# Kernel tuning notes

Measured on AMD Instinct MI355X. Metric: run time of the kernel, lower is better.

Reference implementation:

```python
import jax, jax.numpy as jnp
import numpy as np

N_NODES = 102400
N_EDGES = 1638400
DIMS = [128, 64, 32, 1]  # decoder_dim=128, decoder_l=3, last layer -> 1


def setup_inputs() -> dict:
    key = jax.random.key(0)
    ks = jax.random.split(key, 10)
    inp = {
        'b_z': jax.random.normal(ks[0], (N_NODES, DIMS[0]), jnp.float32),
        'src': jax.random.randint(ks[1], (N_EDGES,), 0, N_NODES, jnp.int64 if jax.config.jax_enable_x64 else jnp.int32),
        'dst': jax.random.randint(ks[2], (N_EDGES,), 0, N_NODES, jnp.int64 if jax.config.jax_enable_x64 else jnp.int32),
        'edge_weight': jax.random.uniform(ks[3], (N_EDGES,), jnp.float32),
        'b_size': 100,
    }
    # GraphConv weights: W [in, out], bias [out] (DGL xavier init; randn ok for ref)
    for i in range(3):
        inp[f'W{i}'] = jax.random.normal(ks[4 + i], (DIMS[i], DIMS[i + 1]), jnp.float32) * (1.0 / np.sqrt(DIMS[i]))
        inp[f'b{i}'] = jnp.zeros((DIMS[i + 1],), jnp.float32)
    return inp


def _gcn_layer(h, src, dst, ew, W, b, activate):
    n = h.shape[0]
    ones = jnp.ones((src.shape[0],), h.dtype)
    # norm='both': symmetric degree normalization with plain (unweighted) degrees
    out_deg = jnp.clip(jax.ops.segment_sum(ones, src, num_segments=n), 1.0)
    in_deg = jnp.clip(jax.ops.segment_sum(ones, dst, num_segments=n), 1.0)
    h = h * (out_deg ** -0.5)[:, None]
    h = h @ W  # in_feats > out_feats: transform before aggregation (DGL order)
    msg = h[src] * ew[:, None]           # [E, out] edge-weighted gather
    agg = jax.ops.segment_sum(msg, dst, num_segments=n)  # scatter-add
    agg = agg * (in_deg ** -0.5)[:, None] + b
    return jnp.tanh(agg) if activate else agg


def reference(b_z, src, dst, edge_weight, b_size, W0, b0, W1, b1, W2, b2):
    h = b_z
    h = _gcn_layer(h, src, dst, edge_weight, W0, b0, True)
    h = _gcn_layer(h, src, dst, edge_weight, W1, b1, True)
    h = _gcn_layer(h, src, dst, edge_weight, W2, b2, False)
    return h.reshape(b_size, -1)
```

## Files before the change

### kernel.cpp

```cpp
#include <hip/hip_runtime.h>
#include <hip/hip_fp16.h>
#include <math.h>

#define N_NODES 102400
#define N_EDGES 1638400
#define NB 100
#define PB 256
#define EPB (N_EDGES/PB)

union H4 { int2 i2; __half h[4]; };

__global__ __launch_bounds__(256) void histA_kernel(const int* __restrict__ src, const int* __restrict__ dst,
                                                    int* __restrict__ histD, int* __restrict__ histS) {
    __shared__ int hD[NB], hS[NB];
    int tid = threadIdx.x;
    if (tid < NB) { hD[tid] = 0; hS[tid] = 0; }
    __syncthreads();
    int base = blockIdx.x * EPB;
    for (int i = tid; i < EPB; i += 256) {
        atomicAdd(&hD[dst[base + i] >> 10], 1);
        atomicAdd(&hS[src[base + i] >> 10], 1);
    }
    __syncthreads();
    if (tid < NB) {
        histD[blockIdx.x * NB + tid] = hD[tid];
        histS[blockIdx.x * NB + tid] = hS[tid];
    }
}

__global__ __launch_bounds__(256) void scanB_kernel(const int* __restrict__ histD, const int* __restrict__ histS,
                                                    int* __restrict__ offD, int* __restrict__ offS,
                                                    int* __restrict__ coarseD, int* __restrict__ coarseS) {
    __shared__ int totD[NB], totS[NB], baseD[NB + 1], baseS[NB + 1];
    int t = threadIdx.x;
    if (t < NB) { int s = 0; for (int k = 0; k < PB; k++) s += histD[k * NB + t]; totD[t] = s; }
    else if (t >= 128 && t < 128 + NB) { int j = t - 128; int s = 0; for (int k = 0; k < PB; k++) s += histS[k * NB + j]; totS[j] = s; }
    __syncthreads();
    if (t == 0)   { int r = 0; for (int j = 0; j < NB; j++) { baseD[j] = r; r += totD[j]; } baseD[NB] = r; }
    if (t == 128) { int r = 0; for (int j = 0; j < NB; j++) { baseS[j] = r; r += totS[j]; } baseS[NB] = r; }
    __syncthreads();
    if (t < NB) { int r = baseD[t]; for (int k = 0; k < PB; k++) { offD[k * NB + t] = r; r += histD[k * NB + t]; } }
    else if (t >= 128 && t < 128 + NB) { int j = t - 128; int r = baseS[j]; for (int k = 0; k < PB; k++) { offS[k * NB + j] = r; r += histS[k * NB + j]; } }
    if (t <= NB) coarseD[t] = baseD[t];
    if (t >= 128 && t <= 128 + NB) coarseS[t - 128] = baseS[t - 128];
}

__global__ __launch_bounds__(256) void partC_kernel(const int* __restrict__ src, const int* __restrict__ dst,
                                                    const float* __restrict__ ew,
                                                    const int* __restrict__ offD, const int* __restrict__ offS,
                                                    int2* __restrict__ partD, unsigned short* __restrict__ partS) {
    __shared__ int cD[NB], cS[NB];
    int tid = threadIdx.x;
    if (tid < NB) { cD[tid] = offD[blockIdx.x * NB + tid]; cS[tid] = offS[blockIdx.x * NB + tid]; }
    __syncthreads();
    int base = blockIdx.x * EPB;
    for (int i = tid; i < EPB; i += 256) {
        int s = src[base + i], d = dst[base + i];
        float w = ew[base + i];
        int p = atomicAdd(&cD[d >> 10], 1);
        partD[p] = make_int2(s | ((d & 1023) << 17), __float_as_int(w));
        int q = atomicAdd(&cS[s >> 10], 1);
        partS[q] = (unsigned short)(s & 1023);
    }
}

__global__ __launch_bounds__(1024) void fineS_kernel(const unsigned short* __restrict__ partS, const int* __restrict__ coarseS,
                                                     float* __restrict__ outdeg_inv) {
    __shared__ int hist[1024];
    int tid = threadIdx.x;
    hist[tid] = 0;
    __syncthreads();
    int beg = coarseS[blockIdx.x], end = coarseS[blockIdx.x + 1];
    for (int i = beg + tid; i < end; i += 1024) atomicAdd(&hist[partS[i]], 1);
    __syncthreads();
    outdeg_inv[blockIdx.x * 1024 + tid] = 1.0f / sqrtf((float)max(hist[tid], 1));
}

__global__ __launch_bounds__(1024) void fineD_kernel(const int2* __restrict__ partD, const int* __restrict__ coarseD,
                                                     const float* __restrict__ outdeg_inv,
                                                     int2* __restrict__ edge_perm, int* __restrict__ row_off,
                                                     float* __restrict__ indeg_inv) {
    __shared__ int hist[1024], cursor[1024];
    __shared__ int wsum[16];
    int tid = threadIdx.x, lane = tid & 63, wid = tid >> 6;
    hist[tid] = 0;
    __syncthreads();
    int beg = coarseD[blockIdx.x], end = coarseD[blockIdx.x + 1];
    for (int i = beg + tid; i < end; i += 1024) atomicAdd(&hist[(partD[i].x >> 17) & 1023], 1);
    __syncthreads();
    int v = hist[tid];
    int x = v;
    #pragma unroll
    for (int s = 1; s < 64; s <<= 1) { int t = __shfl_up(x, s, 64); if (lane >= s) x += t; }
    if (lane == 63) wsum[wid] = x;
    __syncthreads();
    if (wid == 0) {
        int ws = (lane < 16) ? wsum[lane] : 0;
        int y = ws;
        #pragma unroll
        for (int s = 1; s < 16; s <<= 1) { int t = __shfl_up(y, s, 64); if (lane >= s) y += t; }
        if (lane < 16) wsum[lane] = y - ws;
    }
    __syncthreads();
    int ex = wsum[wid] + x - v;
    cursor[tid] = beg + ex;
    int node = blockIdx.x * 1024 + tid;
    row_off[node] = beg + ex;
    indeg_inv[node] = 1.0f / sqrtf((float)max(v, 1));
    if (blockIdx.x == NB - 1 && tid == 0) row_off[N_NODES] = N_EDGES;
    __syncthreads();
    for (int i = beg + tid; i < end; i += 1024) {
        int2 t2 = partD[i];
        int d = (t2.x >> 17) & 1023, s = t2.x & 0x1FFFF;
        int p = atomicAdd(&cursor[d], 1);
        float w = __int_as_float(t2.y) * outdeg_inv[s];
        edge_perm[p] = make_int2(s, __float_as_int(w));
    }
}

template<int K, int C, int RN>
__global__ __launch_bounds__(256) void gemm_tile_kernel(
    const float* __restrict__ h, const float* __restrict__ W, __half* __restrict__ out) {
    constexpr int BM = 64;
    constexpr int RM = 4;
    constexpr int KC = 64;
    constexpr int TX = C / RN;
    constexpr int TY = BM / RM;
    static_assert(TX * TY == 256, "bad tile");
    static_assert(RN == 4, "fp16 epilogue assumes RN==4");

    __shared__ float Ws[K * C];
    __shared__ float Hs[KC][BM + 4];

    const int tid = threadIdx.x;
    const long brow = (long)blockIdx.x * BM;

    for (int i = tid; i < K * C; i += 256) Ws[i] = W[i];

    const int tx = tid % TX;
    const int ty = tid / TX;
    float acc[RM][RN] = {};

    const int lr = tid % 16;
    const int lk = tid / 16;

    for (int kc = 0; kc < K; kc += KC) {
        __syncthreads();
        #pragma unroll
        for (int p0 = 0; p0 < BM; p0 += 16) {
            const int r = p0 + lr;
            const float4 hv = *(const float4*)(h + (brow + r) * K + kc + lk * 4);
            Hs[lk * 4 + 0][r] = hv.x;
            Hs[lk * 4 + 1][r] = hv.y;
            Hs[lk * 4 + 2][r] = hv.z;
            Hs[lk * 4 + 3][r] = hv.w;
        }
        __syncthreads();

        #pragma unroll
        for (int k = 0; k < KC; ++k) {
            const float4 a4 = *(const float4*)&Hs[k][ty * RM];
            const float av[RM] = {a4.x, a4.y, a4.z, a4.w};
            float b[RN];
            *(float4*)b = *(const float4*)&Ws[(kc + k) * C + tx * RN];
            #pragma unroll
            for (int i = 0; i < RM; ++i)
                #pragma unroll
                for (int j = 0; j < RN; ++j)
                    acc[i][j] += av[i] * b[j];
        }
    }

    #pragma unroll
    for (int i = 0; i < RM; ++i) {
        const long row = brow + ty * RM + i;
        __half2 p01 = __floats2half2_rn(acc[i][0], acc[i][1]);
        __half2 p23 = __floats2half2_rn(acc[i][2], acc[i][3]);
        int2 packed = make_int2(*(int*)&p01, *(int*)&p23);
        *(int2*)(out + row * C + tx * RN) = packed;
    }
}

__global__ __launch_bounds__(256) void agg64_gemm_kernel(
    const __half* __restrict__ ht, const int* __restrict__ row_off,
    const int2* __restrict__ ep, const float* __restrict__ indeg_inv,
    const float* __restrict__ b0, const float* __restrict__ W1,
    __half* __restrict__ ht1, int N) {
    __shared__ float h1s[8][64];
    const int tid = threadIdx.x;
    const int lane = tid & 63;
    const int wv = tid >> 6;
    const int chunk = lane & 15;
    const int eslot = lane >> 4;
    const int hf = lane >> 5;
    const int c = lane & 31;

    float w1reg[32];
    #pragma unroll
    for (int j = 0; j < 32; ++j) w1reg[j] = W1[(hf * 32 + j) * 32 + c];
    const float bch = b0[(chunk << 2) | eslot];
    const char* htb = (const char*)ht;
    const unsigned coff = (unsigned)(chunk << 3);

    const int pair0 = (blockIdx.x * blockDim.x + tid) >> 6;
    const int npairs = N >> 1;
    const int nwaves = (gridDim.x * blockDim.x) >> 6;

    for (int pid = pair0; pid < npairs; pid += nwaves) {
        const int n0 = pid << 1;
        const int ro0 = row_off[n0], ro1 = row_off[n0 + 1], ro2 = row_off[n0 + 2];
        const int em0 = max(ro1 - 1, 0), em1 = max(ro2 - 1, 0);
        float4 a0 = {0, 0, 0, 0}, a1 = {0, 0, 0, 0};
        float4 c0 = {0, 0, 0, 0}, c1 = {0, 0, 0, 0};
        int e0 = ro0, e1 = ro1;
        while (true) {
            const int i00 = e0 + eslot, i01 = i00 + 4, i02 = i00 + 8, i03 = i00 + 12;
            const int j00 = e1 + eslot, j01 = j00 + 4, j02 = j00 + 8, j03 = j00 + 12;
            int2 p00 = ep[min(i00, em0)];
            int2 p01 = ep[min(i01, em0)];
            int2 p02 = ep[min(i02, em0)];
            int2 p03 = ep[min(i03, em0)];
            int2 p10 = ep[min(j00, em1)];
            int2 p11 = ep[min(j01, em1)];
            int2 p12 = ep[min(j02, em1)];
            int2 p13 = ep[min(j03, em1)];
            float w00 = (i00 < ro1) ? __int_as_float(p00.y) : 0.0f;
            float w01 = (i01 < ro1) ? __int_as_float(p01.y) : 0.0f;
            float w02 = (i02 < ro1) ? __int_as_float(p02.y) : 0.0f;
            float w03 = (i03 < ro1) ? __int_as_float(p03.y) : 0.0f;
            float w10 = (j00 < ro2) ? __int_as_float(p10.y) : 0.0f;
            float w11 = (j01 < ro2) ? __int_as_float(p11.y) : 0.0f;
            float w12 = (j02 < ro2) ? __int_as_float(p12.y) : 0.0f;
            float w13 = (j03 < ro2) ? __int_as_float(p13.y) : 0.0f;
            H4 r00, r01, r02, r03, r10, r11, r12, r13;
            r00.i2 = *(const int2*)(htb + (((unsigned)p00.x << 7) | coff));
            r01.i2 = *(const int2*)(htb + (((unsigned)p01.x << 7) | coff));
            r02.i2 = *(const int2*)(htb + (((unsigned)p02.x << 7) | coff));
            r03.i2 = *(const int2*)(htb + (((unsigned)p03.x << 7) | coff));
            r10.i2 = *(const int2*)(htb + (((unsigned)p10.x << 7) | coff));
            r11.i2 = *(const int2*)(htb + (((unsigned)p11.x << 7) | coff));
            r12.i2 = *(const int2*)(htb + (((unsigned)p12.x << 7) | coff));
            r13.i2 = *(const int2*)(htb + (((unsigned)p13.x << 7) | coff));
            a0.x = fmaf(__half2float(r00.h[0]), w00, a0.x);
            a0.y = fmaf(__half2float(r00.h[1]), w00, a0.y);
            a0.z = fmaf(__half2float(r00.h[2]), w00, a0.z);
            a0.w = fmaf(__half2float(r00.h[3]), w00, a0.w);
            a1.x = fmaf(__half2float(r01.h[0]), w01, a1.x);
            a1.y = fmaf(__half2float(r01.h[1]), w01, a1.y);
            a1.z = fmaf(__half2float(r01.h[2]), w01, a1.z);
            a1.w = fmaf(__half2float(r01.h[3]), w01, a1.w);
            a0.x = fmaf(__half2float(r02.h[0]), w02, a0.x);
            a0.y = fmaf(__half2float(r02.h[1]), w02, a0.y);
            a0.z = fmaf(__half2float(r02.h[2]), w02, a0.z);
            a0.w = fmaf(__half2float(r02.h[3]), w02, a0.w);
            a1.x = fmaf(__half2float(r03.h[0]), w03, a1.x);
            a1.y = fmaf(__half2float(r03.h[1]), w03, a1.y);
            a1.z = fmaf(__half2float(r03.h[2]), w03, a1.z);
            a1.w = fmaf(__half2float(r03.h[3]), w03, a1.w);
            c0.x = fmaf(__half2float(r10.h[0]), w10, c0.x);
            c0.y = fmaf(__half2float(r10.h[1]), w10, c0.y);
            c0.z = fmaf(__half2float(r10.h[2]), w10, c0.z);
            c0.w = fmaf(__half2float(r10.h[3]), w10, c0.w);
            c1.x = fmaf(__half2float(r11.h[0]), w11, c1.x);
            c1.y = fmaf(__half2float(r11.h[1]), w11, c1.y);
            c1.z = fmaf(__half2float(r11.h[2]), w11, c1.z);
            c1.w = fmaf(__half2float(r11.h[3]), w11, c1.w);
            c0.x = fmaf(__half2float(r12.h[0]), w12, c0.x);
            c0.y = fmaf(__half2float(r12.h[1]), w12, c0.y);
            c0.z = fmaf(__half2float(r12.h[2]), w12, c0.z);
            c0.w = fmaf(__half2float(r12.h[3]), w12, c0.w);
            c1.x = fmaf(__half2float(r13.h[0]), w13, c1.x);
            c1.y = fmaf(__half2float(r13.h[1]), w13, c1.y);
            c1.z = fmaf(__half2float(r13.h[2]), w13, c1.z);
            c1.w = fmaf(__half2float(r13.h[3]), w13, c1.w);
            e0 += 16; e1 += 16;
            if (e0 >= ro1 && e1 >= ro2) break;
        }
        a0.x += a1.x; a0.y += a1.y; a0.z += a1.z; a0.w += a1.w;
        c0.x += c1.x; c0.y += c1.y; c0.z += c1.z; c0.w += c1.w;
        #pragma unroll
        for (int s = 16; s <= 32; s <<= 1) {
            a0.x += __shfl_xor(a0.x, s, 64);
            a0.y += __shfl_xor(a0.y, s, 64);
            a0.z += __shfl_xor(a0.z, s, 64);
            a0.w += __shfl_xor(a0.w, s, 64);
            c0.x += __shfl_xor(c0.x, s, 64);
            c0.y += __shfl_xor(c0.y, s, 64);
            c0.z += __shfl_xor(c0.z, s, 64);
            c0.w += __shfl_xor(c0.w, s, 64);
        }
        const float sc0 = indeg_inv[n0], sc1 = indeg_inv[n0 + 1];
        float v0 = (eslot == 0) ? a0.x : (eslot == 1) ? a0.y : (eslot == 2) ? a0.z : a0.w;
        float v1 = (eslot == 0) ? c0.x : (eslot == 1) ? c0.y : (eslot == 2) ? c0.z : c0.w;
        v0 = tanhf(fmaf(v0, sc0, bch));
        v1 = tanhf(fmaf(v1, sc1, bch));
        const int sl = wv << 1;
        h1s[sl][(chunk << 2) | eslot] = v0;
        h1s[sl + 1][(chunk << 2) | eslot] = v1;
        asm volatile("s_waitcnt lgkmcnt(0)" ::: "memory");
        float t0 = 0.0f, t1 = 0.0f;
        #pragma unroll
        for (int j4 = 0; j4 < 8; ++j4) {
            const float4 h0 = *(const float4*)&h1s[sl][hf * 32 + j4 * 4];
            const float4 h1 = *(const float4*)&h1s[sl + 1][hf * 32 + j4 * 4];
            t0 = fmaf(h0.x, w1reg[j4 * 4 + 0], t0);
            t0 = fmaf(h0.y, w1reg[j4 * 4 + 1], t0);
            t0 = fmaf(h0.z, w1reg[j4 * 4 + 2], t0);
            t0 = fmaf(h0.w, w1reg[j4 * 4 + 3], t0);
            t1 = fmaf(h1.x, w1reg[j4 * 4 + 0], t1);
            t1 = fmaf(h1.y, w1reg[j4 * 4 + 1], t1);
            t1 = fmaf(h1.z, w1reg[j4 * 4 + 2], t1);
            t1 = fmaf(h1.w, w1reg[j4 * 4 + 3], t1);
        }
        t0 += __shfl_xor(t0, 32, 64);
        t1 += __shfl_xor(t1, 32, 64);
        if (hf == 0) {
            ht1[(long)n0 * 32 + c] = __float2half_rn(t0);
            ht1[(long)(n0 + 1) * 32 + c] = __float2half_rn(t1);
        }
    }
}

__global__ __launch_bounds__(256) void agg32_dot_kernel(const __half* __restrict__ ht, const int* __restrict__ row_off,
                                 const int2* __restrict__ ep,
                                 const float* __restrict__ indeg_inv, const float* __restrict__ bias,
                                 const float* __restrict__ W2, float* __restrict__ ht2, int N) {
    int pid = (blockIdx.x * blockDim.x + threadIdx.x) >> 6;
    int lane = threadIdx.x & 63;
    int n0 = pid << 1;
    if (n0 >= N) return;
    int chunk = lane & 7;
    int eslot = lane >> 3;
    int ro0 = row_off[n0], ro1 = row_off[n0 + 1], ro2 = row_off[n0 + 2];
    int em0 = max(ro1 - 1, 0), em1 = max(ro2 - 1, 0);
    const char* htb = (const char*)ht;
    unsigned coff = (unsigned)(chunk << 3);
    float4 a0 = {0, 0, 0, 0}, a1 = {0, 0, 0, 0};
    float4 c0 = {0, 0, 0, 0}, c1 = {0, 0, 0, 0};
    int e0 = ro0, e1 = ro1;
    while (true) {
        int i00 = e0 + eslot, i01 = i00 + 8;
        int j00 = e1 + eslot, j01 = j00 + 8;
        int2 p00 = ep[min(i00, em0)];
        int2 p01 = ep[min(i01, em0)];
        int2 p10 = ep[min(j00, em1)];
        int2 p11 = ep[min(j01, em1)];
        float w00 = (i00 < ro1) ? __int_as_float(p00.y) : 0.0f;
        float w01 = (i01 < ro1) ? __int_as_float(p01.y) : 0.0f;
        float w10 = (j00 < ro2) ? __int_as_float(p10.y) : 0.0f;
        float w11 = (j01 < ro2) ? __int_as_float(p11.y) : 0.0f;
        H4 r00, r01, r10, r11;
        r00.i2 = *(const int2*)(htb + (((unsigned)p00.x << 6) | coff));
        r01.i2 = *(const int2*)(htb + (((unsigned)p01.x << 6) | coff));
        r10.i2 = *(const int2*)(htb + (((unsigned)p10.x << 6) | coff));
        r11.i2 = *(const int2*)(htb + (((unsigned)p11.x << 6) | coff));
        a0.x = fmaf(__half2float(r00.h[0]), w00, a0.x);
        a0.y = fmaf(__half2float(r00.h[1]), w00, a0.y);
        a0.z = fmaf(__half2float(r00.h[2]), w00, a0.z);
        a0.w = fmaf(__half2float(r00.h[3]), w00, a0.w);
        a1.x = fmaf(__half2float(r01.h[0]), w01, a1.x);
        a1.y = fmaf(__half2float(r01.h[1]), w01, a1.y);
        a1.z = fmaf(__half2float(r01.h[2]), w01, a1.z);
        a1.w = fmaf(__half2float(r01.h[3]), w01, a1.w);
        c0.x = fmaf(__half2float(r10.h[0]), w10, c0.x);
        c0.y = fmaf(__half2float(r10.h[1]), w10, c0.y);
        c0.z = fmaf(__half2float(r10.h[2]), w10, c0.z);
        c0.w = fmaf(__half2float(r10.h[3]), w10, c0.w);
        c1.x = fmaf(__half2float(r11.h[0]), w11, c1.x);
        c1.y = fmaf(__half2float(r11.h[1]), w11, c1.y);
        c1.z = fmaf(__half2float(r11.h[2]), w11, c1.z);
        c1.w = fmaf(__half2float(r11.h[3]), w11, c1.w);
        e0 += 16; e1 += 16;
        if (e0 >= ro1 && e1 >= ro2) break;
    }
    a0.x += a1.x; a0.y += a1.y; a0.z += a1.z; a0.w += a1.w;
    c0.x += c1.x; c0.y += c1.y; c0.z += c1.z; c0.w += c1.w;
    #pragma unroll
    for (int s = 8; s <= 32; s <<= 1) {
        a0.x += __shfl_xor(a0.x, s, 64);
        a0.y += __shfl_xor(a0.y, s, 64);
        a0.z += __shfl_xor(a0.z, s, 64);
        a0.w += __shfl_xor(a0.w, s, 64);
        c0.x += __shfl_xor(c0.x, s, 64);
        c0.y += __shfl_xor(c0.y, s, 64);
        c0.z += __shfl_xor(c0.z, s, 64);
        c0.w += __shfl_xor(c0.w, s, 64);
    }
    int q = eslot & 3;
    int ch = (chunk << 2) | q;
    float bb = bias[ch], ww = W2[ch];
    float sc0 = indeg_inv[n0], sc1 = indeg_inv[n0 + 1];
    float v0 = (q == 0) ? a0.x : (q == 1) ? a0.y : (q == 2) ? a0.z : a0.w;
    float v1 = (q == 0) ? c0.x : (q == 1) ? c0.y : (q == 2) ? c0.z : c0.w;
    float t0 = tanhf(fmaf(v0, sc0, bb)) * ww;
    float t1 = tanhf(fmaf(v1, sc1, bb)) * ww;
    #pragma unroll
    for (int s = 1; s <= 32; s <<= 1) {
        t0 += __shfl_xor(t0, s, 64);
        t1 += __shfl_xor(t1, s, 64);
    }
    if (lane == 0) {
        ht2[n0] = 0.5f * t0;
        ht2[n0 + 1] = 0.5f * t1;
    }
}

__global__ void agg1_kernel(const float* __restrict__ ht2, const int* __restrict__ row_off,
                            const int2* __restrict__ ep,
                            const float* __restrict__ indeg_inv, const float* __restrict__ bias,
                            float* __restrict__ out, int N) {
    int wave = (blockIdx.x * blockDim.x + threadIdx.x) >> 6;
    int lane = threadIdx.x & 63;
    int sub = lane >> 4;
    int slot = lane & 15;
    int node = wave * 4 + sub;
    if (node >= N) return;
    int beg = row_off[node], end = row_off[node + 1];
    float acc = 0.0f;
    for (int e = beg + slot; e < end; e += 16) {
        int2 t = ep[e];
        acc += ht2[t.x] * __int_as_float(t.y);
    }
    #pragma unroll
    for (int s = 1; s <= 8; s <<= 1) acc += __shfl_xor(acc, s, 64);
    if (slot == 0) out[node] = acc * indeg_inv[node] + bias[0];
}

extern "C" void kernel_launch(void* const* d_in, const int* in_sizes, int n_in,
                              void* d_out, int out_size, void* d_ws, size_t ws_size,
                              hipStream_t stream) {
    const float* b_z = (const float*)d_in[0];
    const int*   src = (const int*)d_in[1];
    const int*   dst = (const int*)d_in[2];
    const float* ew  = (const float*)d_in[3];
    const float* W0 = (const float*)d_in[5];
    const float* b0 = (const float*)d_in[6];
    const float* W1 = (const float*)d_in[7];
    const float* b1 = (const float*)d_in[8];
    const float* W2 = (const float*)d_in[9];
    const float* b2 = (const float*)d_in[10];
    float* out = (float*)d_out;

    const int N = N_NODES;
    const int E = N_EDGES;

    char* p = (char*)d_ws;
    int*   row_off    = (int*)p;            p += (size_t)(N + 4) * 4;
    float* outdeg_inv = (float*)p;          p += (size_t)N * 4;
    float* indeg_inv  = (float*)p;          p += (size_t)N * 4;
    int*   histD      = (int*)p;            p += (size_t)PB * NB * 4;
    int*   histS      = (int*)p;            p += (size_t)PB * NB * 4;
    int*   offD       = (int*)p;            p += (size_t)PB * NB * 4;
    int*   offS       = (int*)p;            p += (size_t)PB * NB * 4;
    int*   coarseD    = (int*)p;            p += (size_t)(NB + 4) * 4;
    int*   coarseS    = (int*)p;            p += (size_t)(NB + 4) * 4;
    int2*  edge_perm  = (int2*)p;           p += (size_t)E * 8;
    float* bufA       = (float*)p;          p += (size_t)N * 64 * 4;
    float* bufB       = (float*)p;
    int2*           partD = (int2*)bufA;
    unsigned short* partS = (unsigned short*)bufB;
    __half* ht    = (__half*)bufA;
    __half* ht1   = (__half*)bufB;
    float*  ht2   = bufA;

    histA_kernel<<<PB, 256, 0, stream>>>(src, dst, histD, histS);
    scanB_kernel<<<1, 256, 0, stream>>>(histD, histS, offD, offS, coarseD, coarseS);
    partC_kernel<<<PB, 256, 0, stream>>>(src, dst, ew, offD, offS, partD, partS);
    fineS_kernel<<<NB, 1024, 0, stream>>>(partS, coarseS, outdeg_inv);
    fineD_kernel<<<NB, 1024, 0, stream>>>(partD, coarseD, outdeg_inv, edge_perm, row_off, indeg_inv);

    gemm_tile_kernel<128, 64, 4><<<N / 64, 256, 0, stream>>>(b_z, W0, ht);

    agg64_gemm_kernel<<<4096, 256, 0, stream>>>(ht, row_off, edge_perm, indeg_inv, b0, W1, ht1, N);

    agg32_dot_kernel<<<N / 8, 256, 0, stream>>>(ht1, row_off, edge_perm, indeg_inv, b1, W2, ht2, N);

    agg1_kernel<<<N / 16, 256, 0, stream>>>(ht2, row_off, edge_perm, indeg_inv, b2, out, N);
}
```

Baseline: 330.2 us.

## Compute out-degree via global atomics and process four nodes per wave in agg32

Drops the source-side partition and fine histogram kernel. Out-degrees are now counted with global atomics into a zeroed buffer, and partC_kernel converts them to inverse square roots. This removes one kernel launch and the partS scatter traffic, at the cost of contended global atomics. Separately, agg32_dot now gives each wave four destination nodes instead of two, so more gathers are in flight per iteration, using more registers.

```diff
diff --git a/kernel.cpp b/kernel.cpp
--- a/kernel.cpp
+++ b/kernel.cpp
@@ -11,47 +11,43 @@
 union H4 { int2 i2; __half h[4]; };
 
 __global__ __launch_bounds__(256) void histA_kernel(const int* __restrict__ src, const int* __restrict__ dst,
-                                                    int* __restrict__ histD, int* __restrict__ histS) {
-    __shared__ int hD[NB], hS[NB];
+                                                    int* __restrict__ histD, int* __restrict__ outdegCnt) {
+    __shared__ int hD[NB];
     int tid = threadIdx.x;
-    if (tid < NB) { hD[tid] = 0; hS[tid] = 0; }
+    if (tid < NB) hD[tid] = 0;
     __syncthreads();
     int base = blockIdx.x * EPB;
     for (int i = tid; i < EPB; i += 256) {
         atomicAdd(&hD[dst[base + i] >> 10], 1);
-        atomicAdd(&hS[src[base + i] >> 10], 1);
-    }
-    __syncthreads();
-    if (tid < NB) {
-        histD[blockIdx.x * NB + tid] = hD[tid];
-        histS[blockIdx.x * NB + tid] = hS[tid];
-    }
-}
-
-__global__ __launch_bounds__(256) void scanB_kernel(const int* __restrict__ histD, const int* __restrict__ histS,
-                                                    int* __restrict__ offD, int* __restrict__ offS,
-                                                    int* __restrict__ coarseD, int* __restrict__ coarseS) {
-    __shared__ int totD[NB], totS[NB], baseD[NB + 1], baseS[NB + 1];
+        atomicAdd(&outdegCnt[src[base + i]], 1);
+    }
+    __syncthreads();
+    if (tid < NB) histD[blockIdx.x * NB + tid] = hD[tid];
+}
+
+__global__ __launch_bounds__(256) void scanB_kernel(const int* __restrict__ histD,
+                                                    int* __restrict__ offD, int* __restrict__ coarseD) {
+    __shared__ int totD[NB], baseD[NB + 1];
     int t = threadIdx.x;
     if (t < NB) { int s = 0; for (int k = 0; k < PB; k++) s += histD[k * NB + t]; totD[t] = s; }
-    else if (t >= 128 && t < 128 + NB) { int j = t - 128; int s = 0; for (int k = 0; k < PB; k++) s += histS[k * NB + j]; totS[j] = s; }
-    __syncthreads();
-    if (t == 0)   { int r = 0; for (int j = 0; j < NB; j++) { baseD[j] = r; r += totD[j]; } baseD[NB] = r; }
-    if (t == 128) { int r = 0; for (int j = 0; j < NB; j++) { baseS[j] = r; r += totS[j]; } baseS[NB] = r; }
+    __syncthreads();
+    if (t == 0) { int r = 0; for (int j = 0; j < NB; j++) { baseD[j] = r; r += totD[j]; } baseD[NB] = r; }
     __syncthreads();
     if (t < NB) { int r = baseD[t]; for (int k = 0; k < PB; k++) { offD[k * NB + t] = r; r += histD[k * NB + t]; } }
-    else if (t >= 128 && t < 128 + NB) { int j = t - 128; int r = baseS[j]; for (int k = 0; k < PB; k++) { offS[k * NB + j] = r; r += histS[k * NB + j]; } }
     if (t <= NB) coarseD[t] = baseD[t];
-    if (t >= 128 && t <= 128 + NB) coarseS[t - 128] = baseS[t - 128];
 }
 
 __global__ __launch_bounds__(256) void partC_kernel(const int* __restrict__ src, const int* __restrict__ dst,
                                                     const float* __restrict__ ew,
-                                                    const int* __restrict__ offD, const int* __restrict__ offS,
-                                                    int2* __restrict__ partD, unsigned short* __restrict__ partS) {
-    __shared__ int cD[NB], cS[NB];
+                                                    const int* __restrict__ offD,
+                                                    const int* __restrict__ outdegCnt,
+                                                    float* __restrict__ outdeg_inv,
+                                                    int2* __restrict__ partD) {
+    __shared__ int cD[NB];
     int tid = threadIdx.x;
-    if (tid < NB) { cD[tid] = offD[blockIdx.x * NB + tid]; cS[tid] = offS[blockIdx.x * NB + tid]; }
+    for (int i = blockIdx.x * 256 + tid; i < N_NODES; i += PB * 256)
+        outdeg_inv[i] = 1.0f / sqrtf((float)max(outdegCnt[i], 1));
+    if (tid < NB) cD[tid] = offD[blockIdx.x * NB + tid];
     __syncthreads();
     int base = blockIdx.x * EPB;
     for (int i = tid; i < EPB; i += 256) {
@@ -59,21 +55,7 @@
         float w = ew[base + i];
         int p = atomicAdd(&cD[d >> 10], 1);
         partD[p] = make_int2(s | ((d & 1023) << 17), __float_as_int(w));
-        int q = atomicAdd(&cS[s >> 10], 1);
-        partS[q] = (unsigned short)(s & 1023);
-    }
-}
-
-__global__ __launch_bounds__(1024) void fineS_kernel(const unsigned short* __restrict__ partS, const int* __restrict__ coarseS,
-                                                     float* __restrict__ outdeg_inv) {
-    __shared__ int hist[1024];
-    int tid = threadIdx.x;
-    hist[tid] = 0;
-    __syncthreads();
-    int beg = coarseS[blockIdx.x], end = coarseS[blockIdx.x + 1];
-    for (int i = beg + tid; i < end; i += 1024) atomicAdd(&hist[partS[i]], 1);
-    __syncthreads();
-    outdeg_inv[blockIdx.x * 1024 + tid] = 1.0f / sqrtf((float)max(hist[tid], 1));
+    }
 }
 
 __global__ __launch_bounds__(1024) void fineD_kernel(const int2* __restrict__ partD, const int* __restrict__ coarseD,
@@ -325,35 +307,53 @@
                                  const int2* __restrict__ ep,
                                  const float* __restrict__ indeg_inv, const float* __restrict__ bias,
                                  const float* __restrict__ W2, float* __restrict__ ht2, int N) {
-    int pid = (blockIdx.x * blockDim.x + threadIdx.x) >> 6;
+    int quad = (blockIdx.x * blockDim.x + threadIdx.x) >> 6;
     int lane = threadIdx.x & 63;
-    int n0 = pid << 1;
+    int n0 = quad << 2;
     if (n0 >= N) return;
     int chunk = lane & 7;
     int eslot = lane >> 3;
     int ro0 = row_off[n0], ro1 = row_off[n0 + 1], ro2 = row_off[n0 + 2];
+    int ro3 = row_off[n0 + 3], ro4 = row_off[n0 + 4];
     int em0 = max(ro1 - 1, 0), em1 = max(ro2 - 1, 0);
+    int em2 = max(ro3 - 1, 0), em3 = max(ro4 - 1, 0);
     const char* htb = (const char*)ht;
     unsigned coff = (unsigned)(chunk << 3);
     float4 a0 = {0, 0, 0, 0}, a1 = {0, 0, 0, 0};
+    float4 b0 = {0, 0, 0, 0}, b1 = {0, 0, 0, 0};
     float4 c0 = {0, 0, 0, 0}, c1 = {0, 0, 0, 0};
-    int e0 = ro0, e1 = ro1;
-    while (true) {
+    float4 d0 = {0, 0, 0, 0}, d1 = {0, 0, 0, 0};
+    int e0 = ro0, e1 = ro1, e2 = ro2, e3 = ro3;
+    while (e0 < ro1 || e1 < ro2 || e2 < ro3 || e3 < ro4) {
         int i00 = e0 + eslot, i01 = i00 + 8;
-        int j00 = e1 + eslot, j01 = j00 + 8;
+        int i10 = e1 + eslot, i11 = i10 + 8;
+        int i20 = e2 + eslot, i21 = i20 + 8;
+        int i30 = e3 + eslot, i31 = i30 + 8;
         int2 p00 = ep[min(i00, em0)];
         int2 p01 = ep[min(i01, em0)];
-        int2 p10 = ep[min(j00, em1)];
-        int2 p11 = ep[min(j01, em1)];
+        int2 p10 = ep[min(i10, em1)];
+        int2 p11 = ep[min(i11, em1)];
+        int2 p20 = ep[min(i20, em2)];
+        int2 p21 = ep[min(i21, em2)];
+        int2 p30 = ep[min(i30, em3)];
+        int2 p31 = ep[min(i31, em3)];
         float w00 = (i00 < ro1) ? __int_as_float(p00.y) : 0.0f;
         float w01 = (i01 < ro1) ? __int_as_float(p01.y) : 0.0f;
-        float w10 = (j00 < ro2) ? __int_as_float(p10.y) : 0.0f;
-        float w11 = (j01 < ro2) ? __int_as_float(p11.y) : 0.0f;
-        H4 r00, r01, r10, r11;
+        float w10 = (i10 < ro2) ? __int_as_float(p10.y) : 0.0f;
+        float w11 = (i11 < ro2) ? __int_as_float(p11.y) : 0.0f;
+        float w20 = (i20 < ro3) ? __int_as_float(p20.y) : 0.0f;
+        float w21 = (i21 < ro3) ? __int_as_float(p21.y) : 0.0f;
+        float w30 = (i30 < ro4) ? __int_as_float(p30.y) : 0.0f;
+        float w31 = (i31 < ro4) ? __int_as_float(p31.y) : 0.0f;
+        H4 r00, r01, r10, r11, r20, r21, r30, r31;
         r00.i2 = *(const int2*)(htb + (((unsigned)p00.x << 6) | coff));
         r01.i2 = *(const int2*)(htb + (((unsigned)p01.x << 6) | coff));
         r10.i2 = *(const int2*)(htb + (((unsigned)p10.x << 6) | coff));
         r11.i2 = *(const int2*)(htb + (((unsigned)p11.x << 6) | coff));
+        r20.i2 = *(const int2*)(htb + (((unsigned)p20.x << 6) | coff));
+        r21.i2 = *(const int2*)(htb + (((unsigned)p21.x << 6) | coff));
+        r30.i2 = *(const int2*)(htb + (((unsigned)p30.x << 6) | coff));
+        r31.i2 = *(const int2*)(htb + (((unsigned)p31.x << 6) | coff));
         a0.x = fmaf(__half2float(r00.h[0]), w00, a0.x);
         a0.y = fmaf(__half2float(r00.h[1]), w00, a0.y);
         a0.z = fmaf(__half2float(r00.h[2]), w00, a0.z);
@@ -362,46 +362,79 @@
         a1.y = fmaf(__half2float(r01.h[1]), w01, a1.y);
         a1.z = fmaf(__half2float(r01.h[2]), w01, a1.z);
         a1.w = fmaf(__half2float(r01.h[3]), w01, a1.w);
-        c0.x = fmaf(__half2float(r10.h[0]), w10, c0.x);
-        c0.y = fmaf(__half2float(r10.h[1]), w10, c0.y);
-        c0.z = fmaf(__half2float(r10.h[2]), w10, c0.z);
-        c0.w = fmaf(__half2float(r10.h[3]), w10, c0.w);
-        c1.x = fmaf(__half2float(r11.h[0]), w11, c1.x);
-        c1.y = fmaf(__half2float(r11.h[1]), w11, c1.y);
-        c1.z = fmaf(__half2float(r11.h[2]), w11, c1.z);
-        c1.w = fmaf(__half2float(r11.h[3]), w11, c1.w);
-        e0 += 16; e1 += 16;
-        if (e0 >= ro1 && e1 >= ro2) break;
+        b0.x = fmaf(__half2float(r10.h[0]), w10, b0.x);
+        b0.y = fmaf(__half2float(r10.h[1]), w10, b0.y);
+        b0.z = fmaf(__half2float(r10.h[2]), w10, b0.z);
+        b0.w = fmaf(__half2float(r10.h[3]), w10, b0.w);
+        b1.x = fmaf(__half2float(r11.h[0]), w11, b1.x);
+        b1.y = fmaf(__half2float(r11.h[1]), w11, b1.y);
+        b1.z = fmaf(__half2float(r11.h[2]), w11, b1.z);
+        b1.w = fmaf(__half2float(r11.h[3]), w11, b1.w);
+        c0.x = fmaf(__half2float(r20.h[0]), w20, c0.x);
+        c0.y = fmaf(__half2float(r20.h[1]), w20, c0.y);
+        c0.z = fmaf(__half2float(r20.h[2]), w20, c0.z);
+        c0.w = fmaf(__half2float(r20.h[3]), w20, c0.w);
+        c1.x = fmaf(__half2float(r21.h[0]), w21, c1.x);
+        c1.y = fmaf(__half2float(r21.h[1]), w21, c1.y);
+        c1.z = fmaf(__half2float(r21.h[2]), w21, c1.z);
+        c1.w = fmaf(__half2float(r21.h[3]), w21, c1.w);
+        d0.x = fmaf(__half2float(r30.h[0]), w30, d0.x);
+        d0.y = fmaf(__half2float(r30.h[1]), w30, d0.y);
+        d0.z = fmaf(__half2float(r30.h[2]), w30, d0.z);
+        d0.w = fmaf(__half2float(r30.h[3]), w30, d0.w);
+        d1.x = fmaf(__half2float(r31.h[0]), w31, d1.x);
+        d1.y = fmaf(__half2float(r31.h[1]), w31, d1.y);
+        d1.z = fmaf(__half2float(r31.h[2]), w31, d1.z);
+        d1.w = fmaf(__half2float(r31.h[3]), w31, d1.w);
+        e0 += 16; e1 += 16; e2 += 16; e3 += 16;
     }
     a0.x += a1.x; a0.y += a1.y; a0.z += a1.z; a0.w += a1.w;
+    b0.x += b1.x; b0.y += b1.y; b0.z += b1.z; b0.w += b1.w;
     c0.x += c1.x; c0.y += c1.y; c0.z += c1.z; c0.w += c1.w;
+    d0.x += d1.x; d0.y += d1.y; d0.z += d1.z; d0.w += d1.w;
     #pragma unroll
     for (int s = 8; s <= 32; s <<= 1) {
         a0.x += __shfl_xor(a0.x, s, 64);
         a0.y += __shfl_xor(a0.y, s, 64);
         a0.z += __shfl_xor(a0.z, s, 64);
         a0.w += __shfl_xor(a0.w, s, 64);
+        b0.x += __shfl_xor(b0.x, s, 64);
+        b0.y += __shfl_xor(b0.y, s, 64);
+        b0.z += __shfl_xor(b0.z, s, 64);
+        b0.w += __shfl_xor(b0.w, s, 64);
         c0.x += __shfl_xor(c0.x, s, 64);
         c0.y += __shfl_xor(c0.y, s, 64);
         c0.z += __shfl_xor(c0.z, s, 64);
         c0.w += __shfl_xor(c0.w, s, 64);
+        d0.x += __shfl_xor(d0.x, s, 64);
+        d0.y += __shfl_xor(d0.y, s, 64);
+        d0.z += __shfl_xor(d0.z, s, 64);
+        d0.w += __shfl_xor(d0.w, s, 64);
     }
     int q = eslot & 3;
     int ch = (chunk << 2) | q;
     float bb = bias[ch], ww = W2[ch];
-    float sc0 = indeg_inv[n0], sc1 = indeg_inv[n0 + 1];
+    float s0 = indeg_inv[n0], s1 = indeg_inv[n0 + 1], s2 = indeg_inv[n0 + 2], s3 = indeg_inv[n0 + 3];
     float v0 = (q == 0) ? a0.x : (q == 1) ? a0.y : (q == 2) ? a0.z : a0.w;
-    float v1 = (q == 0) ? c0.x : (q == 1) ? c0.y : (q == 2) ? c0.z : c0.w;
-    float t0 = tanhf(fmaf(v0, sc0, bb)) * ww;
-    float t1 = tanhf(fmaf(v1, sc1, bb)) * ww;
+    float v1 = (q == 0) ? b0.x : (q == 1) ? b0.y : (q == 2) ? b0.z : b0.w;
+    float v2 = (q == 0) ? c0.x : (q == 1) ? c0.y : (q == 2) ? c0.z : c0.w;
+    float v3 = (q == 0) ? d0.x : (q == 1) ? d0.y : (q == 2) ? d0.z : d0.w;
+    float t0 = tanhf(fmaf(v0, s0, bb)) * ww;
+    float t1 = tanhf(fmaf(v1, s1, bb)) * ww;
+    float t2 = tanhf(fmaf(v2, s2, bb)) * ww;
+    float t3 = tanhf(fmaf(v3, s3, bb)) * ww;
     #pragma unroll
     for (int s = 1; s <= 32; s <<= 1) {
         t0 += __shfl_xor(t0, s, 64);
         t1 += __shfl_xor(t1, s, 64);
+        t2 += __shfl_xor(t2, s, 64);
+        t3 += __shfl_xor(t3, s, 64);
     }
     if (lane == 0) {
         ht2[n0] = 0.5f * t0;
         ht2[n0 + 1] = 0.5f * t1;
+        ht2[n0 + 2] = 0.5f * t2;
+        ht2[n0 + 3] = 0.5f * t3;
     }
 }
 
@@ -449,31 +482,28 @@
     float* outdeg_inv = (float*)p;          p += (size_t)N * 4;
     float* indeg_inv  = (float*)p;          p += (size_t)N * 4;
     int*   histD      = (int*)p;            p += (size_t)PB * NB * 4;
-    int*   histS      = (int*)p;            p += (size_t)PB * NB * 4;
     int*   offD       = (int*)p;            p += (size_t)PB * NB * 4;
-    int*   offS       = (int*)p;            p += (size_t)PB * NB * 4;
     int*   coarseD    = (int*)p;            p += (size_t)(NB + 4) * 4;
-    int*   coarseS    = (int*)p;            p += (size_t)(NB + 4) * 4;
     int2*  edge_perm  = (int2*)p;           p += (size_t)E * 8;
     float* bufA       = (float*)p;          p += (size_t)N * 64 * 4;
     float* bufB       = (float*)p;
-    int2*           partD = (int2*)bufA;
-    unsigned short* partS = (unsigned short*)bufB;
+    int2*   partD     = (int2*)bufA;
+    int*    outdegCnt = (int*)bufB;
     __half* ht    = (__half*)bufA;
     __half* ht1   = (__half*)bufB;
     float*  ht2   = bufA;
 
-    histA_kernel<<<PB, 256, 0, stream>>>(src, dst, histD, histS);
-    scanB_kernel<<<1, 256, 0, stream>>>(histD, histS, offD, offS, coarseD, coarseS);
-    partC_kernel<<<PB, 256, 0, stream>>>(src, dst, ew, offD, offS, partD, partS);
-    fineS_kernel<<<NB, 1024, 0, stream>>>(partS, coarseS, outdeg_inv);
+    hipMemsetAsync(outdegCnt, 0, (size_t)N * 4, stream);
+    histA_kernel<<<PB, 256, 0, stream>>>(src, dst, histD, outdegCnt);
+    scanB_kernel<<<1, 256, 0, stream>>>(histD, offD, coarseD);
+    partC_kernel<<<PB, 256, 0, stream>>>(src, dst, ew, offD, outdegCnt, outdeg_inv, partD);
     fineD_kernel<<<NB, 1024, 0, stream>>>(partD, coarseD, outdeg_inv, edge_perm, row_off, indeg_inv);
 
     gemm_tile_kernel<128, 64, 4><<<N / 64, 256, 0, stream>>>(b_z, W0, ht);
 
     agg64_gemm_kernel<<<4096, 256, 0, stream>>>(ht, row_off, edge_perm, indeg_inv, b0, W1, ht1, N);
 
-    agg32_dot_kernel<<<N / 8, 256, 0, stream>>>(ht1, row_off, edge_perm, indeg_inv, b1, W2, ht2, N);
+    agg32_dot_kernel<<<N / 16, 256, 0, stream>>>(ht1, row_off, edge_perm, indeg_inv, b1, W2, ht2, N);
 
     agg1_kernel<<<N / 16, 256, 0, stream>>>(ht2, row_off, edge_perm, indeg_inv, b2, out, N);
 }
```

New measurement: 374.8 us. 1.14x slower.
